# Kernel tuning notes

Measured on AMD Instinct MI355X. Metric: run time of the kernel, lower is better.

## Reference

```python
import jax, jax.numpy as jnp
import numpy as np

N, K = 8192, 16          # nodes, neighbours per node
FEAT = 128               # size + 1 (attention input dim)
DIST = 128               # distance_size (query dim & block width)
H, D = 8, 128            # heads, per-head attention size
HID = 128                # MLP hidden size
SCALE = 1.0 / np.sqrt(D)


def _lin_init(k, i, o):
    return jax.random.normal(k, (i, o), jnp.float32) / np.sqrt(i)


def setup_inputs() -> dict:
    key = jax.random.key(0)
    ks = jax.random.split(key, 12)
    z = lambda n: jnp.zeros((n,), jnp.float32)
    return {
        "features": jax.random.normal(ks[0], (N, FEAT), jnp.float32),
        "distance_features": jax.random.normal(ks[1], (N, DIST), jnp.float32),
        "structure": jax.random.randint(ks[2], (N, K), 0, N, jnp.int32),
        # attention projections
        "Wq": _lin_init(ks[3], DIST, H * D), "bq": z(H * D),
        "Wk": _lin_init(ks[4], FEAT, H * D), "bk": z(H * D),
        "Wv": _lin_init(ks[5], FEAT, H * D), "bv": z(H * D),
        "Wo": _lin_init(ks[6], H * D, DIST), "bo": z(DIST),
        # local MLP: depth=3 hidden layers + output layer
        "W1": _lin_init(ks[7], DIST, HID), "b1": z(HID),
        "W2": _lin_init(ks[8], HID, HID), "b2": z(HID),
        "W3": _lin_init(ks[9], HID, HID), "b3": z(HID),
        "W4": _lin_init(ks[10], HID, DIST), "b4": z(DIST),
    }


def reference(features, distance_features, structure,
              Wq, bq, Wk, bk, Wv, bv, Wo, bo,
              W1, b1, W2, b2, W3, b3, W4, b4):
    # bn / local_bn are identity (batch_norm=False); dropout identity (eval)
    normed = distance_features

    # NeighbourDotMultiHeadAttention: queries from distance feats, K/V from node feats
    q = (normed @ Wq + bq).reshape(N, H, D)
    k = (features @ Wk + bk).reshape(N, H, D)
    v = (features @ Wv + bv).reshape(N, H, D)
    kg = k[structure]                                  # [N, K, H, D] neighbour keys
    vg = v[structure]                                  # [N, K, H, D] neighbour values
    logits = jnp.einsum('nhd,nkhd->nkh', q, kg) * SCALE
    attn = jax.nn.softmax(logits, axis=1)              # over K neighbours
    att = jnp.einsum('nkh,nkhd->nhd', attn, vg).reshape(N, H * D)
    att_out = att @ Wo + bo                            # [N, DIST]

    out = distance_features + att_out                  # residual 1

    # local MLP with relu activations
    h = jax.nn.relu(out @ W1 + b1)
    h = jax.nn.relu(h @ W2 + b2)
    h = jax.nn.relu(h @ W3 + b3)
    mlp = h @ W4 + b4

    return out + mlp                                   # residual 2
```

## Files before the change

kernel.cpp:

```cpp
#include <hip/hip_runtime.h>
#include <hip/hip_bf16.h>

typedef float f32x4 __attribute__((ext_vector_type(4)));
typedef short s16x8 __attribute__((ext_vector_type(8)));
typedef _Float16 h8v __attribute__((ext_vector_type(8)));
typedef _Float16 h4v __attribute__((ext_vector_type(4)));
typedef _Float16 h2v __attribute__((ext_vector_type(2)));
typedef unsigned short u16;

#define N_NODES 8192
#define KNBR 16
#define SCALE 0.08838834764831845f

__device__ __forceinline__ float bf2f(u16 h) {
    unsigned v = ((unsigned)h) << 16;
    return __builtin_bit_cast(float, v);
}
__device__ __forceinline__ u16 f2bf(float f) {
    __hip_bfloat16 h = __float2bfloat16(f);
    return __builtin_bit_cast(u16, h);
}
__device__ __forceinline__ u16 f2h(float f) {
    _Float16 h = (_Float16)f;
    return __builtin_bit_cast(u16, h);
}

__global__ void prep_kernel(const float* __restrict__ feat, const float* __restrict__ dist,
                            const float* __restrict__ Wq, const float* __restrict__ Wk,
                            const float* __restrict__ Wv, const float* __restrict__ Wo,
                            const float* __restrict__ W1, const float* __restrict__ W2,
                            const float* __restrict__ W3, const float* __restrict__ W4,
                            const float* __restrict__ bq, const float* __restrict__ bk,
                            const float* __restrict__ bv,
                            u16* __restrict__ featb, u16* __restrict__ distb,
                            u16* __restrict__ Wqkvt, u16* __restrict__ Wot,
                            u16* __restrict__ Wmlpt, float* __restrict__ bqkv) {
    int gid = blockIdx.x * 256 + threadIdx.x;
    featb[gid] = f2bf(feat[gid]);
    distb[gid] = f2bf(dist[gid]);
    if (gid < 3072 * 128) {
        int col = gid >> 7, k = gid & 127;
        float v = (col < 1024) ? Wq[k * 1024 + col]
                : (col < 2048) ? Wk[k * 1024 + (col - 1024)]
                               : Wv[k * 1024 + (col - 2048)];
        Wqkvt[gid] = f2bf(v);
    }
    if (gid < 128 * 1024) {
        int col = gid >> 10, k = gid & 1023;
        Wot[gid] = f2bf(Wo[k * 128 + col]);
    }
    if (gid < 4 * 128 * 128) {
        int m = gid >> 14, r = gid & 16383;
        int col = r >> 7, k = r & 127;
        const float* Wm = (m == 0) ? W1 : (m == 1) ? W2 : (m == 2) ? W3 : W4;
        Wmlpt[gid] = f2bf(Wm[k * 128 + col]);
    }
    if (gid < 3072) {
        bqkv[gid] = (gid < 1024) ? bq[gid] : (gid < 2048) ? bk[gid - 1024] : bv[gid - 2048];
    }
}

__global__ __launch_bounds__(256, 2) void qkv_gemm(const u16* __restrict__ featb,
                                                   const u16* __restrict__ distb,
                                                   const u16* __restrict__ Wqkvt,
                                                   const float* __restrict__ bqkv,
                                                   u16* __restrict__ qkvh) {
    const int rt = blockIdx.x, ct = blockIdx.y;
    const int w = threadIdx.x >> 6, l = threadIdx.x & 63;
    const int rbase = rt * 256 + w * 64;
    const int cbase = ct * 128;
    const u16* A = (ct < 8) ? distb : featb;

    s16x8 af[4][4];
#pragma unroll
    for (int mf = 0; mf < 4; mf++) {
        const u16* ar = A + (size_t)(rbase + mf * 16 + (l & 15)) * 128 + ((l >> 4) * 8);
#pragma unroll
        for (int kk = 0; kk < 4; kk++) af[mf][kk] = *(const s16x8*)(ar + kk * 32);
    }

    f32x4 acc[4][8];
#pragma unroll
    for (int mf = 0; mf < 4; mf++)
#pragma unroll
        for (int nf = 0; nf < 8; nf++) acc[mf][nf] = (f32x4){0.f, 0.f, 0.f, 0.f};

#pragma unroll
    for (int nf = 0; nf < 8; nf++) {
        const u16* bp = Wqkvt + (size_t)(cbase + nf * 16 + (l & 15)) * 128 + ((l >> 4) * 8);
        s16x8 b0 = *(const s16x8*)bp;
        s16x8 b1 = *(const s16x8*)(bp + 32);
        s16x8 b2 = *(const s16x8*)(bp + 64);
        s16x8 b3 = *(const s16x8*)(bp + 96);
#pragma unroll
        for (int mf = 0; mf < 4; mf++) {
            acc[mf][nf] = __builtin_amdgcn_mfma_f32_16x16x32_bf16(af[mf][0], b0, acc[mf][nf], 0, 0, 0);
            acc[mf][nf] = __builtin_amdgcn_mfma_f32_16x16x32_bf16(af[mf][1], b1, acc[mf][nf], 0, 0, 0);
            acc[mf][nf] = __builtin_amdgcn_mfma_f32_16x16x32_bf16(af[mf][2], b2, acc[mf][nf], 0, 0, 0);
            acc[mf][nf] = __builtin_amdgcn_mfma_f32_16x16x32_bf16(af[mf][3], b3, acc[mf][nf], 0, 0, 0);
        }
    }

    float bias[8];
#pragma unroll
    for (int nf = 0; nf < 8; nf++) bias[nf] = bqkv[cbase + nf * 16 + (l & 15)];

    u16* obase = qkvh + ((size_t)ct * 8192 + rbase) * 128 + (l & 15);
#pragma unroll
    for (int mf = 0; mf < 4; mf++) {
#pragma unroll
        for (int nf = 0; nf < 8; nf++) {
#pragma unroll
            for (int r = 0; r < 4; r++) {
                const int row = mf * 16 + (l >> 4) * 4 + r;
                obase[(size_t)row * 128 + nf * 16] = f2h(acc[mf][nf][r] + bias[nf]);
            }
        }
    }
}

__global__ __launch_bounds__(256) void attn_kernel(const u16* __restrict__ qkvh,
                                                   const int* __restrict__ structure,
                                                   u16* __restrict__ attb) {
    const int head = blockIdx.x & 7, chunk = blockIdx.x >> 3;
    const int w = threadIdx.x >> 6, l = threadIdx.x & 63;
    const int ni = l >> 3, lh = l & 7;
    const int n = chunk * 32 + w * 8 + ni;

    const _Float16* qtab = (const _Float16*)qkvh;
    const _Float16* qrow = qtab + ((size_t)head * 8192 + n) * 128 + lh * 16;
    h8v q0 = *(const h8v*)qrow;
    h8v q1 = *(const h8v*)(qrow + 8);

    const int2 idx2 = ((const int2*)structure)[n * 8 + lh];
    const _Float16* kbase = qtab + (size_t)(8 + head) * 8192 * 128;
    const _Float16* vbase = qtab + (size_t)(16 + head) * 8192 * 128;

    float logit[16];
#pragma unroll
    for (int half = 0; half < 2; half++) {
        h8v kd0[8], kd1[8];
#pragma unroll
        for (int j8 = 0; j8 < 8; j8++) {
            const int j = half * 8 + j8;
            int idx = __shfl(j & 1 ? idx2.y : idx2.x, (ni << 3) | (j >> 1));
            const _Float16* krow = kbase + (size_t)idx * 128 + lh * 16;
            kd0[j8] = *(const h8v*)krow;
            kd1[j8] = *(const h8v*)(krow + 8);
        }
#pragma unroll
        for (int j8 = 0; j8 < 8; j8++) {
            h8v a = kd0[j8] * q0 + kd1[j8] * q1;
            h4v a4 = a.lo + a.hi;
            h2v a2 = a4.lo + a4.hi;
            float s = (float)a2.x + (float)a2.y;
            s += __shfl_xor(s, 1);
            s += __shfl_xor(s, 2);
            s += __shfl_xor(s, 4);
            logit[half * 8 + j8] = s * SCALE;
        }
    }

    float m = logit[0];
#pragma unroll
    for (int j = 1; j < 16; j++) m = fmaxf(m, logit[j]);
    float sum = 0.f;
#pragma unroll
    for (int j = 0; j < 16; j++) { logit[j] = __expf(logit[j] - m); sum += logit[j]; }
    const float inv = 1.f / sum;

    h8v acc0 = (h8v)((_Float16)0.f);
    h8v acc1 = (h8v)((_Float16)0.f);
#pragma unroll
    for (int half = 0; half < 2; half++) {
        h8v vd0[8], vd1[8];
#pragma unroll
        for (int j8 = 0; j8 < 8; j8++) {
            const int j = half * 8 + j8;
            int idx = __shfl(j & 1 ? idx2.y : idx2.x, (ni << 3) | (j >> 1));
            const _Float16* vrow = vbase + (size_t)idx * 128 + lh * 16;
            vd0[j8] = *(const h8v*)vrow;
            vd1[j8] = *(const h8v*)(vrow + 8);
        }
#pragma unroll
        for (int j8 = 0; j8 < 8; j8++) {
            const _Float16 p = (_Float16)(logit[half * 8 + j8] * inv);
            acc0 += vd0[j8] * p;
            acc1 += vd1[j8] * p;
        }
    }

    s16x8 o0, o1;
#pragma unroll
    for (int t = 0; t < 8; t++) {
        o0[t] = (short)f2bf((float)acc0[t]);
        o1[t] = (short)f2bf((float)acc1[t]);
    }
    u16* orow = attb + (size_t)n * 1024 + head * 128 + lh * 16;
    *(s16x8*)orow = o0;
    *(s16x8*)(orow + 8) = o1;
}

__global__ __launch_bounds__(128) void out_mlp(const u16* __restrict__ attb,
                                               const u16* __restrict__ Wot,
                                               const u16* __restrict__ Wmlpt,
                                               const float* __restrict__ dist,
                                               const float* __restrict__ bo,
                                               const float* __restrict__ b1,
                                               const float* __restrict__ b2,
                                               const float* __restrict__ b3,
                                               const float* __restrict__ b4,
                                               float* __restrict__ out) {
    __shared__ __attribute__((aligned(16))) u16 act[2][16][136];
    const int w = threadIdx.x >> 6, l = threadIdx.x & 63;
    const int rbase = blockIdx.x * 16;
    const int cb = w * 64;

    f32x4 acc[4];
#pragma unroll
    for (int i = 0; i < 4; i++) acc[i] = (f32x4){0.f, 0.f, 0.f, 0.f};

    const u16* ap = attb + (size_t)(rbase + (l & 15)) * 1024 + ((l >> 4) * 8);
#pragma unroll 8
    for (int kk = 0; kk < 32; kk++) {
        s16x8 af = *(const s16x8*)(ap + kk * 32);
#pragma unroll
        for (int nf = 0; nf < 4; nf++) {
            const u16* bp = Wot + (size_t)(cb + nf * 16 + (l & 15)) * 1024 + kk * 32 + ((l >> 4) * 8);
            s16x8 bf = *(const s16x8*)bp;
            acc[nf] = __builtin_amdgcn_mfma_f32_16x16x32_bf16(af, bf, acc[nf], 0, 0, 0);
        }
    }

    float outsave[4][4];
#pragma unroll
    for (int nf = 0; nf < 4; nf++) {
        const int gcol = cb + nf * 16 + (l & 15);
        const float bv = bo[gcol];
#pragma unroll
        for (int r = 0; r < 4; r++) {
            const int rl = (l >> 4) * 4 + r;
            float v = acc[nf][r] + bv + dist[(size_t)(rbase + rl) * 128 + gcol];
            outsave[nf][r] = v;
            act[0][rl][gcol] = f2bf(v);
        }
    }
    __syncthreads();

#pragma unroll
    for (int layer = 0; layer < 4; layer++) {
        const int rd = layer & 1, wr = (layer + 1) & 1;
        f32x4 macc[4];
#pragma unroll
        for (int i = 0; i < 4; i++) macc[i] = (f32x4){0.f, 0.f, 0.f, 0.f};
#pragma unroll
        for (int kk = 0; kk < 4; kk++) {
            s16x8 af = *(const s16x8*)&act[rd][l & 15][kk * 32 + ((l >> 4) * 8)];
#pragma unroll
            for (int nf = 0; nf < 4; nf++) {
                const u16* bp = Wmlpt + layer * 16384
                              + (size_t)(cb + nf * 16 + (l & 15)) * 128 + kk * 32 + ((l >> 4) * 8);
                s16x8 bf = *(const s16x8*)bp;
                macc[nf] = __builtin_amdgcn_mfma_f32_16x16x32_bf16(af, bf, macc[nf], 0, 0, 0);
            }
        }
        const float* bias = (layer == 0) ? b1 : (layer == 1) ? b2 : (layer == 2) ? b3 : b4;
        if (layer < 3) {
#pragma unroll
            for (int nf = 0; nf < 4; nf++) {
                const int gcol = cb + nf * 16 + (l & 15);
                const float bv = bias[gcol];
#pragma unroll
                for (int r = 0; r < 4; r++) {
                    const int rl = (l >> 4) * 4 + r;
                    act[wr][rl][gcol] = f2bf(fmaxf(macc[nf][r] + bv, 0.f));
                }
            }
            __syncthreads();
        } else {
#pragma unroll
            for (int nf = 0; nf < 4; nf++) {
                const int gcol = cb + nf * 16 + (l & 15);
                const float bv = bias[gcol];
#pragma unroll
                for (int r = 0; r < 4; r++) {
                    const int rl = (l >> 4) * 4 + r;
                    out[(size_t)(rbase + rl) * 128 + gcol] = outsave[nf][r] + macc[nf][r] + bv;
                }
            }
        }
    }
}

extern "C" void kernel_launch(void* const* d_in, const int* in_sizes, int n_in,
                              void* d_out, int out_size, void* d_ws, size_t ws_size,
                              hipStream_t stream) {
    const float* features = (const float*)d_in[0];
    const float* dist     = (const float*)d_in[1];
    const int*   structure= (const int*)d_in[2];
    const float* Wq = (const float*)d_in[3];  const float* bq = (const float*)d_in[4];
    const float* Wk = (const float*)d_in[5];  const float* bk = (const float*)d_in[6];
    const float* Wv = (const float*)d_in[7];  const float* bv = (const float*)d_in[8];
    const float* Wo = (const float*)d_in[9];  const float* bo = (const float*)d_in[10];
    const float* W1 = (const float*)d_in[11]; const float* b1 = (const float*)d_in[12];
    const float* W2 = (const float*)d_in[13]; const float* b2 = (const float*)d_in[14];
    const float* W3 = (const float*)d_in[15]; const float* b3 = (const float*)d_in[16];
    const float* W4 = (const float*)d_in[17]; const float* b4 = (const float*)d_in[18];
    float* out = (float*)d_out;

    u16* wsp   = (u16*)d_ws;
    u16* qkvh  = wsp;
    u16* attb  = qkvh  + (size_t)3 * 8 * 8192 * 128;
    u16* featb = attb  + (size_t)8192 * 1024;
    u16* distb = featb + (size_t)8192 * 128;
    u16* Wqkvt = distb + (size_t)8192 * 128;
    u16* Wot   = Wqkvt + (size_t)3072 * 128;
    u16* Wmlpt = Wot   + (size_t)128 * 1024;
    float* bqkv = (float*)(Wmlpt + (size_t)4 * 128 * 128);

    prep_kernel<<<4096, 256, 0, stream>>>(features, dist, Wq, Wk, Wv, Wo, W1, W2, W3, W4,
                                          bq, bk, bv, featb, distb, Wqkvt, Wot, Wmlpt, bqkv);
    qkv_gemm<<<dim3(32, 24), 256, 0, stream>>>(featb, distb, Wqkvt, bqkv, qkvh);
    attn_kernel<<<2048, 256, 0, stream>>>(qkvh, structure, attb);
    out_mlp<<<512, 128, 0, stream>>>(attb, Wot, Wmlpt, dist, bo, b1, b2, b3, b4, out);
}
```

Baseline: 189.4 us.

## Split out-projection K dimension across four waves with LDS reduction in out_mlp

The out_mlp kernel now runs 4 waves per block instead of 2. Each wave computes a partial out-projection over a quarter of the 1024-wide K dimension, covering all 128 output columns. The partials are reduced through shared memory, with the residual and bias added in a vectorised pass. This raises parallelism and memory-level parallelism on the long K loop for the 512-block grid. The cost is more LDS use (about 40KB per block), an extra barrier and reduction pass, and MLP layers that each wave computes with only 32 columns.

Result: no change. 188.3 us (-0.6%).

```diff
diff --git a/kernel.cpp b/kernel.cpp
--- a/kernel.cpp
+++ b/kernel.cpp
@@ -201,7 +201,7 @@
     *(s16x8*)(orow + 8) = o1;
 }
 
-__global__ __launch_bounds__(128) void out_mlp(const u16* __restrict__ attb,
+__global__ __launch_bounds__(256) void out_mlp(const u16* __restrict__ attb,
                                                const u16* __restrict__ Wot,
                                                const u16* __restrict__ Wmlpt,
                                                const float* __restrict__ dist,
@@ -211,64 +211,92 @@
                                                const float* __restrict__ b3,
                                                const float* __restrict__ b4,
                                                float* __restrict__ out) {
+    __shared__ __attribute__((aligned(16))) float part[4][16][128];
+    __shared__ __attribute__((aligned(16))) float outf[16][128];
     __shared__ __attribute__((aligned(16))) u16 act[2][16][136];
     const int w = threadIdx.x >> 6, l = threadIdx.x & 63;
     const int rbase = blockIdx.x * 16;
-    const int cb = w * 64;
-
-    f32x4 acc[4];
-#pragma unroll
-    for (int i = 0; i < 4; i++) acc[i] = (f32x4){0.f, 0.f, 0.f, 0.f};
-
-    const u16* ap = attb + (size_t)(rbase + (l & 15)) * 1024 + ((l >> 4) * 8);
-#pragma unroll 8
-    for (int kk = 0; kk < 32; kk++) {
-        s16x8 af = *(const s16x8*)(ap + kk * 32);
-#pragma unroll
-        for (int nf = 0; nf < 4; nf++) {
-            const u16* bp = Wot + (size_t)(cb + nf * 16 + (l & 15)) * 1024 + kk * 32 + ((l >> 4) * 8);
-            s16x8 bf = *(const s16x8*)bp;
-            acc[nf] = __builtin_amdgcn_mfma_f32_16x16x32_bf16(af, bf, acc[nf], 0, 0, 0);
-        }
-    }
-
-    float outsave[4][4];
-#pragma unroll
-    for (int nf = 0; nf < 4; nf++) {
-        const int gcol = cb + nf * 16 + (l & 15);
-        const float bv = bo[gcol];
+
+    f32x4 acc[8];
+#pragma unroll
+    for (int i = 0; i < 8; i++) acc[i] = (f32x4){0.f, 0.f, 0.f, 0.f};
+
+    const u16* ap = attb + (size_t)(rbase + (l & 15)) * 1024 + w * 256 + ((l >> 4) * 8);
+    s16x8 af[8];
+#pragma unroll
+    for (int kk = 0; kk < 8; kk++) af[kk] = *(const s16x8*)(ap + kk * 32);
+
+#pragma unroll
+    for (int nf = 0; nf < 8; nf++) {
+        const u16* bp = Wot + (size_t)(nf * 16 + (l & 15)) * 1024 + w * 256 + ((l >> 4) * 8);
+        s16x8 bf[8];
+#pragma unroll
+        for (int kk = 0; kk < 8; kk++) bf[kk] = *(const s16x8*)(bp + kk * 32);
+#pragma unroll
+        for (int kk = 0; kk < 8; kk++)
+            acc[nf] = __builtin_amdgcn_mfma_f32_16x16x32_bf16(af[kk], bf[kk], acc[nf], 0, 0, 0);
+    }
+
+#pragma unroll
+    for (int nf = 0; nf < 8; nf++) {
+        const int gcol = nf * 16 + (l & 15);
 #pragma unroll
         for (int r = 0; r < 4; r++) {
-            const int rl = (l >> 4) * 4 + r;
-            float v = acc[nf][r] + bv + dist[(size_t)(rbase + rl) * 128 + gcol];
-            outsave[nf][r] = v;
-            act[0][rl][gcol] = f2bf(v);
+            part[w][(l >> 4) * 4 + r][gcol] = acc[nf][r];
         }
     }
     __syncthreads();
 
+    {
+        const int tid = threadIdx.x;
+        const int row = tid >> 4, col0 = (tid & 15) * 8;
+        f32x4 s0 = *(const f32x4*)&part[0][row][col0];
+        f32x4 s1 = *(const f32x4*)&part[0][row][col0 + 4];
+#pragma unroll
+        for (int ww = 1; ww < 4; ww++) {
+            s0 += *(const f32x4*)&part[ww][row][col0];
+            s1 += *(const f32x4*)&part[ww][row][col0 + 4];
+        }
+        const float* dp = dist + (size_t)(rbase + row) * 128 + col0;
+        f32x4 d0 = *(const f32x4*)dp;
+        f32x4 d1 = *(const f32x4*)(dp + 4);
+        f32x4 bo0 = *(const f32x4*)(bo + col0);
+        f32x4 bo1 = *(const f32x4*)(bo + col0 + 4);
+        s0 += d0 + bo0;
+        s1 += d1 + bo1;
+        *(f32x4*)&outf[row][col0] = s0;
+        *(f32x4*)&outf[row][col0 + 4] = s1;
+#pragma unroll
+        for (int e = 0; e < 4; e++) {
+            act[0][row][col0 + e] = f2bf(s0[e]);
+            act[0][row][col0 + 4 + e] = f2bf(s1[e]);
+        }
+    }
+    __syncthreads();
+
+    const int cw = w * 32;
 #pragma unroll
     for (int layer = 0; layer < 4; layer++) {
         const int rd = layer & 1, wr = (layer + 1) & 1;
-        f32x4 macc[4];
-#pragma unroll
-        for (int i = 0; i < 4; i++) macc[i] = (f32x4){0.f, 0.f, 0.f, 0.f};
+        f32x4 macc[2];
+        macc[0] = (f32x4){0.f, 0.f, 0.f, 0.f};
+        macc[1] = (f32x4){0.f, 0.f, 0.f, 0.f};
 #pragma unroll
         for (int kk = 0; kk < 4; kk++) {
-            s16x8 af = *(const s16x8*)&act[rd][l & 15][kk * 32 + ((l >> 4) * 8)];
-#pragma unroll
-            for (int nf = 0; nf < 4; nf++) {
+            s16x8 af2 = *(const s16x8*)&act[rd][l & 15][kk * 32 + ((l >> 4) * 8)];
+#pragma unroll
+            for (int nf = 0; nf < 2; nf++) {
                 const u16* bp = Wmlpt + layer * 16384
-                              + (size_t)(cb + nf * 16 + (l & 15)) * 128 + kk * 32 + ((l >> 4) * 8);
+                              + (size_t)(cw + nf * 16 + (l & 15)) * 128 + kk * 32 + ((l >> 4) * 8);
                 s16x8 bf = *(const s16x8*)bp;
-                macc[nf] = __builtin_amdgcn_mfma_f32_16x16x32_bf16(af, bf, macc[nf], 0, 0, 0);
+                macc[nf] = __builtin_amdgcn_mfma_f32_16x16x32_bf16(af2, bf, macc[nf], 0, 0, 0);
             }
         }
         const float* bias = (layer == 0) ? b1 : (layer == 1) ? b2 : (layer == 2) ? b3 : b4;
         if (layer < 3) {
 #pragma unroll
-            for (int nf = 0; nf < 4; nf++) {
-                const int gcol = cb + nf * 16 + (l & 15);
+            for (int nf = 0; nf < 2; nf++) {
+                const int gcol = cw + nf * 16 + (l & 15);
                 const float bv = bias[gcol];
 #pragma unroll
                 for (int r = 0; r < 4; r++) {
@@ -279,13 +307,13 @@
             __syncthreads();
         } else {
 #pragma unroll
-            for (int nf = 0; nf < 4; nf++) {
-                const int gcol = cb + nf * 16 + (l & 15);
+            for (int nf = 0; nf < 2; nf++) {
+                const int gcol = cw + nf * 16 + (l & 15);
                 const float bv = bias[gcol];
 #pragma unroll
                 for (int r = 0; r < 4; r++) {
                     const int rl = (l >> 4) * 4 + r;
-                    out[(size_t)(rbase + rl) * 128 + gcol] = outsave[nf][r] + macc[nf][r] + bv;
+                    out[(size_t)(rbase + rl) * 128 + gcol] = outf[rl][gcol] + macc[nf][r] + bv;
                 }
             }
         }
@@ -322,5 +350,5 @@
                                           bq, bk, bv, featb, distb, Wqkvt, Wot, Wmlpt, bqkv);
     qkv_gemm<<<dim3(32, 24), 256, 0, stream>>>(featb, distb, Wqkvt, bqkv, qkvh);
     attn_kernel<<<2048, 256, 0, stream>>>(qkvh, structure, attb);
-    out_mlp<<<512, 128, 0, stream>>>(attb, Wot, Wmlpt, dist, bo, b1, b2, b3, b4, out);
-}
+    out_mlp<<<512, 256, 0, stream>>>(attb, Wot, Wmlpt, dist, bo, b1, b2, b3, b4, out);
+}
```
